# Performance work log

Hardware: AMD Instinct MI355X
Metric: run time of the kernel (lower is better)

The kernel has to match this reference:

```python
import jax, jax.numpy as jnp
import numpy as np

TEMP = 0.05
EPS = 1e-6


def _l2norm(x):
    return x / jnp.linalg.norm(x, axis=1, keepdims=True)


def setup_inputs() -> dict:
    key = jax.random.key(0)
    k1, k2, k3, k4 = jax.random.split(key, 4)
    B, D = 4096, 768
    return {
        "feat": jax.random.normal(k1, (B, D), dtype=jnp.float32),
        "feat_gen": jax.random.normal(k2, (B, D), dtype=jnp.float32),
        "feat_aug": jax.random.normal(k3, (B, D), dtype=jnp.float32),
        "targets": jax.random.randint(k4, (B,), 0, 100, dtype=jnp.int64),
    }


def reference(feat, feat_gen, feat_aug, targets):
    B = feat.shape[0]
    on = _l2norm(feat)
    gn = _l2norm(feat_gen)
    an = _l2norm(feat_aug)
    # [B, B] exp-similarity matrices
    exp_ori = jnp.exp(on @ on.T / TEMP)
    exp_gen = jnp.exp(on @ gn.T / TEMP)
    exp_aug = jnp.exp(on @ an.T / TEMP)

    same = (targets[:, None] == targets[None, :])  # [B, B] bool, includes diagonal
    same_f = same.astype(exp_ori.dtype)

    # ---- co loss: anchors vs ori+aug columns ----
    oa = exp_ori + exp_aug
    diff_sum_oa = oa.sum(axis=1) - (oa * same_f).sum(axis=1)        # [B]
    denom_co = diff_sum_oa + exp_gen.sum(axis=1) + EPS              # [B]
    term_o = -jnp.log(exp_ori / (exp_ori + denom_co[:, None]) + EPS)
    term_a = -jnp.log(exp_aug / (exp_aug + denom_co[:, None]) + EPS)
    co_loss = ((term_o + term_a) * same_f).sum() / B

    # ---- ad loss: anchors vs gen columns ----
    diff_sum_g = exp_gen.sum(axis=1) - (exp_gen * same_f).sum(axis=1)
    denom_ad = diff_sum_g + exp_aug.sum(axis=1) + exp_ori.sum(axis=1) + EPS
    term_g = -jnp.log(exp_gen / (exp_gen + denom_ad[:, None]) + EPS)
    ad_loss = (term_g * same_f).sum() / B

    return (ad_loss, co_loss)
```

## Files before the change

kernel.cpp:

```cpp
#include <hip/hip_runtime.h>
#include <hip/hip_bf16.h>
#include <math.h>

#define Bn 4096
#define Dd 768
#define SC2 28.85390081777927f
#define EPSF 1e-6f
#define DG 4.8516519541e8f

#define O_S      0
#define O_SMOA   12288
#define O_SMG    16384
#define ZERO_F   20480
#define O_P      20480
#define O_RM     20608
#define LIST_OFF   262144
#define LCAP       (1u << 19)
#define NB_OFF     33554432

typedef __attribute__((ext_vector_type(8))) short sh8;
typedef __attribute__((ext_vector_type(4))) float f32x4;

#define AS1 __attribute__((address_space(1)))
#define AS3 __attribute__((address_space(3)))

static __device__ __forceinline__ void gl_lds16(const void* g, void* l) {
    __builtin_amdgcn_global_load_lds((const AS1 void*)g, (AS3 void*)l, 16, 0, 0);
}

static __device__ __forceinline__ unsigned short f2b(float f) {
    unsigned int u = __float_as_uint(f);
    unsigned int r = (u + 0x7fffu + ((u >> 16) & 1u)) >> 16;
    return (unsigned short)r;
}

__global__ void norm_kernel(const float* f0, const float* f1, const float* f2, unsigned short* nb) {
    int r = blockIdx.x, m = blockIdx.y, tid = threadIdx.x;
    const float* src = (m == 0 ? f0 : (m == 1 ? f1 : f2)) + (size_t)r * Dd;
    float x0 = src[tid], x1 = src[tid + 256], x2 = src[tid + 512];
    float v = x0 * x0 + x1 * x1 + x2 * x2;
    #pragma unroll
    for (int off = 1; off < 64; off <<= 1) v += __shfl_xor(v, off);
    __shared__ float wr[4];
    if ((tid & 63) == 0) wr[tid >> 6] = v;
    __syncthreads();
    float inv = rsqrtf(wr[0] + wr[1] + wr[2] + wr[3]);
    unsigned short* dst = nb + ((size_t)m * Bn + r) * Dd;
    dst[tid] = f2b(x0 * inv);
    dst[tid + 256] = f2b(x1 * inv);
    dst[tid + 512] = f2b(x2 * inv);
}

__launch_bounds__(1024)
__global__ void sort_kernel(const int* tg, unsigned int* I, float* out) {
    float* F = (float*)I;
    __shared__ unsigned int h[128], pb[128], cur[128];
    int tid = threadIdx.x;
    for (int e = tid; e < ZERO_F; e += 1024) F[e] = 0.f;
    if (tid == 0) { out[0] = 0.f; out[1] = 0.f; }
    if (tid < 128) { h[tid] = 0; cur[tid] = 0; }
    __syncthreads();
    for (int e = tid; e < Bn; e += 1024) atomicAdd(&h[tg[e]], 1u);
    __syncthreads();
    if (tid < 128) pb[tid] = h[tid] * h[tid];
    __syncthreads();
    for (int s = 1; s < 128; s <<= 1) {
        unsigned int b = 0;
        if (tid < 128 && tid >= s) b = pb[tid - s];
        __syncthreads();
        if (tid < 128) pb[tid] += b;
        __syncthreads();
    }
    if (tid == 127) I[O_P] = pb[127];
    uint2* RM = (uint2*)(I + O_RM);
    for (int e = tid; e < Bn; e += 1024) {
        int c = tg[e];
        unsigned int r = atomicAdd(&cur[c], 1u);
        unsigned int n = h[c];
        RM[e] = make_uint2((unsigned)c | (r << 8), (pb[c] - n * n) + r * n);
    }
}

__launch_bounds__(256, 2)
__global__ void gemm_rowsum(const unsigned short* nb, char* ws) {
    float* F = (float*)ws;
    const unsigned int* I = (const unsigned int*)ws;
    const uint2* RM = (const uint2*)(I + O_RM);
    int bid = blockIdx.x;
    int sw = (bid & 7) * 128 + (bid >> 3);
    int m0 = (sw >> 5) * 128, n0 = (sw & 31) * 128;
    int tid = threadIdx.x, lane = tid & 63, wave = tid >> 6;
    int wm = (wave >> 1) * 64, wn = (wave & 1) * 64;
    int lid = lane & 15, q = lane >> 4;
    __shared__ __align__(16) unsigned short Asm[128 * 32];
    __shared__ __align__(16) unsigned short Bsm[3][128 * 32];

    int row0 = tid >> 2, ch = tid & 3;
    int cs = (ch ^ ((row0 >> 1) & 3)) * 8;
    const unsigned short* gA  = nb + (size_t)(m0 + row0) * Dd + cs;
    const unsigned short* gB0 = nb + (size_t)(n0 + row0) * Dd + cs;
    const unsigned short* gB1 = gB0 + (size_t)Bn * Dd;
    const unsigned short* gB2 = gB1 + (size_t)Bn * Dd;
    unsigned short* lA0 = &Asm[tid * 8];
    unsigned short* lA1 = &Asm[(tid + 256) * 8];

    int cswz = (q ^ ((lid >> 1) & 3)) * 8;

    f32x4 a0[4][4] = {}, a1[4][4] = {}, a2[4][4] = {};

    for (int kt = 0; kt < 24; ++kt) {
        const unsigned short* pa  = gA  + kt * 32;
        const unsigned short* pb0 = gB0 + kt * 32;
        const unsigned short* pb1 = gB1 + kt * 32;
        const unsigned short* pb2 = gB2 + kt * 32;
        __syncthreads();
        gl_lds16(pa, lA0);
        gl_lds16(pa + (size_t)64 * Dd, lA1);
        gl_lds16(pb0, &Bsm[0][tid * 8]);
        gl_lds16(pb0 + (size_t)64 * Dd, &Bsm[0][(tid + 256) * 8]);
        gl_lds16(pb1, &Bsm[1][tid * 8]);
        gl_lds16(pb1 + (size_t)64 * Dd, &Bsm[1][(tid + 256) * 8]);
        gl_lds16(pb2, &Bsm[2][tid * 8]);
        gl_lds16(pb2 + (size_t)64 * Dd, &Bsm[2][(tid + 256) * 8]);
        __syncthreads();
        sh8 af[4];
        #pragma unroll
        for (int i = 0; i < 4; ++i)
            af[i] = *(const sh8*)&Asm[(wm + i * 16 + lid) * 32 + cswz];
        {
            sh8 bf[4];
            #pragma unroll
            for (int j = 0; j < 4; ++j)
                bf[j] = *(const sh8*)&Bsm[0][(wn + j * 16 + lid) * 32 + cswz];
            #pragma unroll
            for (int i = 0; i < 4; ++i)
                #pragma unroll
                for (int j = 0; j < 4; ++j)
                    a0[i][j] = __builtin_amdgcn_mfma_f32_16x16x32_bf16(af[i], bf[j], a0[i][j], 0, 0, 0);
        }
        {
            sh8 bf[4];
            #pragma unroll
            for (int j = 0; j < 4; ++j)
                bf[j] = *(const sh8*)&Bsm[1][(wn + j * 16 + lid) * 32 + cswz];
            #pragma unroll
            for (int i = 0; i < 4; ++i)
                #pragma unroll
                for (int j = 0; j < 4; ++j)
                    a1[i][j] = __builtin_amdgcn_mfma_f32_16x16x32_bf16(af[i], bf[j], a1[i][j], 0, 0, 0);
        }
        {
            sh8 bf[4];
            #pragma unroll
            for (int j = 0; j < 4; ++j)
                bf[j] = *(const sh8*)&Bsm[2][(wn + j * 16 + lid) * 32 + cswz];
            #pragma unroll
            for (int i = 0; i < 4; ++i)
                #pragma unroll
                for (int j = 0; j < 4; ++j)
                    a2[i][j] = __builtin_amdgcn_mfma_f32_16x16x32_bf16(af[i], bf[j], a2[i][j], 0, 0, 0);
        }
    }

    uint2 rmc[4];
    #pragma unroll
    for (int j = 0; j < 4; ++j) rmc[j] = RM[n0 + wn + j * 16 + lid];
    uint4* Lq = (uint4*)(ws + LIST_OFF);
    #pragma unroll
    for (int i = 0; i < 4; ++i)
        #pragma unroll
        for (int reg = 0; reg < 4; ++reg) {
            int grow = m0 + wm + i * 16 + q * 4 + reg;
            uint2 rm = RM[grow];
            unsigned int trow = rm.x & 255u, rsb = rm.y;
            float rs0 = 0.f, rs1 = 0.f, rs2 = 0.f, msOA = 0.f, msG = 0.f;
            #pragma unroll
            for (int j = 0; j < 4; ++j) {
                int gcol = n0 + wn + j * 16 + lid;
                float x0 = a0[i][j][reg] * SC2;
                float x1 = a1[i][j][reg] * SC2;
                float x2 = a2[i][j][reg] * SC2;
                float e0 = exp2f(x0);
                float e1 = exp2f(x1);
                float e2 = exp2f(x2);
                if (gcol == grow) e0 = 0.f;
                rs0 += e0; rs1 += e1; rs2 += e2;
                if ((rmc[j].x & 255u) == trow) {
                    msOA += e0 + e2;
                    msG  += e1;
                    unsigned int slot = rsb + (rmc[j].x >> 8);
                    if (slot < LCAP)
                        Lq[slot] = make_uint4((unsigned)grow, __float_as_uint(x0),
                                              __float_as_uint(x1), __float_as_uint(x2));
                }
            }
            #pragma unroll
            for (int off = 1; off < 16; off <<= 1) {
                rs0 += __shfl_xor(rs0, off);
                rs1 += __shfl_xor(rs1, off);
                rs2 += __shfl_xor(rs2, off);
                msOA += __shfl_xor(msOA, off);
                msG  += __shfl_xor(msG, off);
            }
            if (lid == 0) {
                atomicAdd(&F[O_S + grow], rs0);
                atomicAdd(&F[O_S + Bn + grow], rs1);
                atomicAdd(&F[O_S + 2 * Bn + grow], rs2);
                atomicAdd(&F[O_SMOA + grow], msOA);
                atomicAdd(&F[O_SMG + grow], msG);
            }
        }
}

__launch_bounds__(256)
__global__ void loss_kernel(char* ws, float* out) {
    float* F = (float*)ws;
    const unsigned int* I = (const unsigned int*)ws;
    const uint4* L = (const uint4*)(ws + LIST_OFF);
    unsigned int n = I[O_P]; if (n > LCAP) n = LCAP;
    float a0 = 0.f, a1 = 0.f;
    unsigned int stride = gridDim.x * 256;
    for (unsigned int idx = blockIdx.x * 256 + threadIdx.x; idx < n; idx += stride) {
        uint4 en = L[idx];
        int i = (int)en.x;
        float son = F[O_S + i], sgen = F[O_S + Bn + i], saug = F[O_S + 2 * Bn + i];
        float dco = (son + saug - F[O_SMOA + i]) + sgen + EPSF;
        float dad = (sgen - F[O_SMG + i]) + saug + son + DG + EPSF;
        float eo = exp2f(__uint_as_float(en.y));
        float eg = exp2f(__uint_as_float(en.z));
        float ea = exp2f(__uint_as_float(en.w));
        a0 += -__logf(eg / (eg + dad) + EPSF);
        a1 += -__logf(eo / (eo + dco) + EPSF) - __logf(ea / (ea + dco) + EPSF);
    }
    #pragma unroll
    for (int off = 1; off < 64; off <<= 1) { a0 += __shfl_xor(a0, off); a1 += __shfl_xor(a1, off); }
    __shared__ float r0[4], r1[4];
    int tid = threadIdx.x;
    if ((tid & 63) == 0) { r0[tid >> 6] = a0; r1[tid >> 6] = a1; }
    __syncthreads();
    if (tid == 0) {
        atomicAdd(&out[0], (r0[0] + r0[1] + r0[2] + r0[3]) * (1.0f / Bn));
        atomicAdd(&out[1], (r1[0] + r1[1] + r1[2] + r1[3]) * (1.0f / Bn));
    }
}

extern "C" void kernel_launch(void* const* d_in, const int* in_sizes, int n_in,
                              void* d_out, int out_size, void* d_ws, size_t ws_size,
                              hipStream_t stream) {
    const float* f0 = (const float*)d_in[0];
    const float* f1 = (const float*)d_in[1];
    const float* f2 = (const float*)d_in[2];
    const int* tg = (const int*)d_in[3];
    char* ws = (char*)d_ws;
    unsigned int* I = (unsigned int*)d_ws;
    unsigned short* nb = (unsigned short*)(ws + NB_OFF);
    float* out = (float*)d_out;

    norm_kernel<<<dim3(Bn, 3), 256, 0, stream>>>(f0, f1, f2, nb);
    sort_kernel<<<1, 1024, 0, stream>>>(tg, I, out);
    gemm_rowsum<<<dim3(1024), 256, 0, stream>>>(nb, ws);
    loss_kernel<<<256, 256, 0, stream>>>(ws, out);
}
```

Baseline: 205.4 us.

## Fuse sort into norm kernel, remap GEMM tiles per XCD, prioritize MFMA

The single-block sort/histogram kernel is folded into the normalization kernel as an extra block, which removes one kernel launch. GEMM block-to-tile mapping is changed so each XCD owns a group of four column tiles across all rows, aiming for better L2 reuse of B tiles. The inner loop preloads B fragments and wraps MFMA groups in sched_barrier and s_setprio to interleave LDS reads with matrix ops. This raises register pressure and shifts which data each XCD shares.

```diff
diff --git a/kernel.cpp b/kernel.cpp
--- a/kernel.cpp
+++ b/kernel.cpp
@@ -34,8 +34,39 @@
     return (unsigned short)r;
 }
 
-__global__ void norm_kernel(const float* f0, const float* f1, const float* f2, unsigned short* nb) {
+__global__ void norm_sort_kernel(const float* f0, const float* f1, const float* f2,
+                                 unsigned short* nb, const int* tg, unsigned int* I,
+                                 float* out) {
     int r = blockIdx.x, m = blockIdx.y, tid = threadIdx.x;
+    if (r == Bn) {
+        if (m != 0) return;
+        float* F = (float*)I;
+        __shared__ unsigned int h[128], pb[128], cur[128];
+        for (int e = tid; e < ZERO_F; e += 256) F[e] = 0.f;
+        if (tid == 0) { out[0] = 0.f; out[1] = 0.f; }
+        if (tid < 128) { h[tid] = 0; cur[tid] = 0; }
+        __syncthreads();
+        for (int e = tid; e < Bn; e += 256) atomicAdd(&h[tg[e]], 1u);
+        __syncthreads();
+        if (tid < 128) pb[tid] = h[tid] * h[tid];
+        __syncthreads();
+        for (int s = 1; s < 128; s <<= 1) {
+            unsigned int b = 0;
+            if (tid < 128 && tid >= s) b = pb[tid - s];
+            __syncthreads();
+            if (tid < 128) pb[tid] += b;
+            __syncthreads();
+        }
+        if (tid == 127) I[O_P] = pb[127];
+        uint2* RM = (uint2*)(I + O_RM);
+        for (int e = tid; e < Bn; e += 256) {
+            int c = tg[e];
+            unsigned int rk = atomicAdd(&cur[c], 1u);
+            unsigned int n = h[c];
+            RM[e] = make_uint2((unsigned)c | (rk << 8), (pb[c] - n * n) + rk * n);
+        }
+        return;
+    }
     const float* src = (m == 0 ? f0 : (m == 1 ? f1 : f2)) + (size_t)r * Dd;
     float x0 = src[tid], x1 = src[tid + 256], x2 = src[tid + 512];
     float v = x0 * x0 + x1 * x1 + x2 * x2;
@@ -51,44 +82,15 @@
     dst[tid + 512] = f2b(x2 * inv);
 }
 
-__launch_bounds__(1024)
-__global__ void sort_kernel(const int* tg, unsigned int* I, float* out) {
-    float* F = (float*)I;
-    __shared__ unsigned int h[128], pb[128], cur[128];
-    int tid = threadIdx.x;
-    for (int e = tid; e < ZERO_F; e += 1024) F[e] = 0.f;
-    if (tid == 0) { out[0] = 0.f; out[1] = 0.f; }
-    if (tid < 128) { h[tid] = 0; cur[tid] = 0; }
-    __syncthreads();
-    for (int e = tid; e < Bn; e += 1024) atomicAdd(&h[tg[e]], 1u);
-    __syncthreads();
-    if (tid < 128) pb[tid] = h[tid] * h[tid];
-    __syncthreads();
-    for (int s = 1; s < 128; s <<= 1) {
-        unsigned int b = 0;
-        if (tid < 128 && tid >= s) b = pb[tid - s];
-        __syncthreads();
-        if (tid < 128) pb[tid] += b;
-        __syncthreads();
-    }
-    if (tid == 127) I[O_P] = pb[127];
-    uint2* RM = (uint2*)(I + O_RM);
-    for (int e = tid; e < Bn; e += 1024) {
-        int c = tg[e];
-        unsigned int r = atomicAdd(&cur[c], 1u);
-        unsigned int n = h[c];
-        RM[e] = make_uint2((unsigned)c | (r << 8), (pb[c] - n * n) + r * n);
-    }
-}
-
 __launch_bounds__(256, 2)
 __global__ void gemm_rowsum(const unsigned short* nb, char* ws) {
     float* F = (float*)ws;
     const unsigned int* I = (const unsigned int*)ws;
     const uint2* RM = (const uint2*)(I + O_RM);
     int bid = blockIdx.x;
-    int sw = (bid & 7) * 128 + (bid >> 3);
-    int m0 = (sw >> 5) * 128, n0 = (sw & 31) * 128;
+    int xcd = bid & 7, local = bid >> 3;
+    int n0 = (xcd * 4 + (local & 3)) * 128;
+    int m0 = (local >> 2) * 128;
     int tid = threadIdx.x, lane = tid & 63, wave = tid >> 6;
     int wm = (wave >> 1) * 64, wn = (wave & 1) * 64;
     int lid = lane & 15, q = lane >> 4;
@@ -123,43 +125,44 @@
         gl_lds16(pb2, &Bsm[2][tid * 8]);
         gl_lds16(pb2 + (size_t)64 * Dd, &Bsm[2][(tid + 256) * 8]);
         __syncthreads();
-        sh8 af[4];
+        sh8 af[4], bf0[4], bf1[4], bf2[4];
         #pragma unroll
         for (int i = 0; i < 4; ++i)
             af[i] = *(const sh8*)&Asm[(wm + i * 16 + lid) * 32 + cswz];
-        {
-            sh8 bf[4];
+        #pragma unroll
+        for (int j = 0; j < 4; ++j)
+            bf0[j] = *(const sh8*)&Bsm[0][(wn + j * 16 + lid) * 32 + cswz];
+        #pragma unroll
+        for (int j = 0; j < 4; ++j)
+            bf1[j] = *(const sh8*)&Bsm[1][(wn + j * 16 + lid) * 32 + cswz];
+        __builtin_amdgcn_sched_barrier(0);
+        __builtin_amdgcn_s_setprio(1);
+        #pragma unroll
+        for (int i = 0; i < 4; ++i)
             #pragma unroll
             for (int j = 0; j < 4; ++j)
-                bf[j] = *(const sh8*)&Bsm[0][(wn + j * 16 + lid) * 32 + cswz];
-            #pragma unroll
-            for (int i = 0; i < 4; ++i)
-                #pragma unroll
-                for (int j = 0; j < 4; ++j)
-                    a0[i][j] = __builtin_amdgcn_mfma_f32_16x16x32_bf16(af[i], bf[j], a0[i][j], 0, 0, 0);
-        }
-        {
-            sh8 bf[4];
+                a0[i][j] = __builtin_amdgcn_mfma_f32_16x16x32_bf16(af[i], bf0[j], a0[i][j], 0, 0, 0);
+        __builtin_amdgcn_s_setprio(0);
+        __builtin_amdgcn_sched_barrier(0);
+        #pragma unroll
+        for (int j = 0; j < 4; ++j)
+            bf2[j] = *(const sh8*)&Bsm[2][(wn + j * 16 + lid) * 32 + cswz];
+        __builtin_amdgcn_sched_barrier(0);
+        __builtin_amdgcn_s_setprio(1);
+        #pragma unroll
+        for (int i = 0; i < 4; ++i)
             #pragma unroll
             for (int j = 0; j < 4; ++j)
-                bf[j] = *(const sh8*)&Bsm[1][(wn + j * 16 + lid) * 32 + cswz];
-            #pragma unroll
-            for (int i = 0; i < 4; ++i)
-                #pragma unroll
-                for (int j = 0; j < 4; ++j)
-                    a1[i][j] = __builtin_amdgcn_mfma_f32_16x16x32_bf16(af[i], bf[j], a1[i][j], 0, 0, 0);
-        }
-        {
-            sh8 bf[4];
+                a1[i][j] = __builtin_amdgcn_mfma_f32_16x16x32_bf16(af[i], bf1[j], a1[i][j], 0, 0, 0);
+        __builtin_amdgcn_s_setprio(0);
+        __builtin_amdgcn_sched_barrier(0);
+        __builtin_amdgcn_s_setprio(1);
+        #pragma unroll
+        for (int i = 0; i < 4; ++i)
             #pragma unroll
             for (int j = 0; j < 4; ++j)
-                bf[j] = *(const sh8*)&Bsm[2][(wn + j * 16 + lid) * 32 + cswz];
-            #pragma unroll
-            for (int i = 0; i < 4; ++i)
-                #pragma unroll
-                for (int j = 0; j < 4; ++j)
-                    a2[i][j] = __builtin_amdgcn_mfma_f32_16x16x32_bf16(af[i], bf[j], a2[i][j], 0, 0, 0);
-        }
+                a2[i][j] = __builtin_amdgcn_mfma_f32_16x16x32_bf16(af[i], bf2[j], a2[i][j], 0, 0, 0);
+        __builtin_amdgcn_s_setprio(0);
     }
 
     uint2 rmc[4];
@@ -256,8 +259,7 @@
     unsigned short* nb = (unsigned short*)(ws + NB_OFF);
     float* out = (float*)d_out;
 
-    norm_kernel<<<dim3(Bn, 3), 256, 0, stream>>>(f0, f1, f2, nb);
-    sort_kernel<<<1, 1024, 0, stream>>>(tg, I, out);
+    norm_sort_kernel<<<dim3(Bn + 1, 3), 256, 0, stream>>>(f0, f1, f2, nb, tg, I, out);
     gemm_rowsum<<<dim3(1024), 256, 0, stream>>>(nb, ws);
     loss_kernel<<<256, 256, 0, stream>>>(ws, out);
 }
```

Result: no change. 201.5 us (-1.9%).
